# Optimization experiments

Hardware: AMD Instinct MI355X
Metric: run time of the kernel (lower is better)

## Reference

```python
import jax, jax.numpy as jnp
import numpy as np

D_MODEL = 1024
N_HEAD = 16
HEAD_DIM = D_MODEL // N_HEAD
B, T = 4, 1024
MIN_KEEP_H, MAX_KEEP_H = 2, 6


def setup_inputs() -> dict:
    key = jax.random.key(0)
    ks = jax.random.split(key, 8)
    x = jax.random.normal(ks[0], (B, T, D_MODEL), dtype=jnp.float32)
    # SignMaskLinear weight: uniform(-1, 1)
    q_w = jax.random.uniform(ks[1], (D_MODEL, D_MODEL), minval=-1.0, maxval=1.0, dtype=jnp.float32)
    # BitGhostLinear weights: randn
    k_w = jax.random.normal(ks[2], (D_MODEL, D_MODEL), dtype=jnp.float32)
    v_w = jax.random.normal(ks[3], (D_MODEL, D_MODEL), dtype=jnp.float32)
    o_w = jax.random.normal(ks[4], (D_MODEL, D_MODEL), dtype=jnp.float32)
    zeros = jnp.zeros((D_MODEL,), dtype=jnp.float32)
    return {"x": x, "q_w": q_w, "q_b": zeros, "k_w": k_w, "k_b": zeros,
            "v_w": v_w, "v_b": zeros, "o_w": o_w, "o_b": zeros}


def _ghost_attention(x, q_w, q_b, k_w, k_b, v_w, v_b, o_w, o_b):
    Bn, Tn, C = x.shape
    H, Dh = N_HEAD, HEAD_DIM
    # SignMaskLinear: effective weight is sign(w) * (w != 0)
    qw_eff = jnp.sign(q_w) * (q_w != 0).astype(x.dtype)
    q = (x @ qw_eff.T + q_b).reshape(Bn, Tn, H, Dh).transpose(0, 2, 1, 3)  # (B,H,T,Dh)
    k = (x @ k_w.T + k_b).reshape(Bn, Tn, H, Dh).transpose(0, 2, 1, 3)
    v = (x @ v_w.T + v_b).reshape(Bn, Tn, H, Dh).transpose(0, 2, 1, 3)
    # RMS-normalize q
    q = q / (jnp.sqrt(jnp.mean(q * q, axis=-1, keepdims=True)) + 1e-6)
    # Per-head top-k sparsification of q by |q| (static keep counts)
    ratios = np.linspace(0.35, 0.15, H)
    keep_counts = np.maximum((ratios * Dh).astype(np.int64), 1)  # trunc like .long()
    q_abs = jnp.abs(q)
    q_sorted = -jnp.sort(-q_abs, axis=-1)  # descending along Dh
    idx = jnp.asarray(keep_counts - 1, dtype=jnp.int32).reshape(1, H, 1, 1)
    thresh = jnp.take_along_axis(q_sorted, jnp.broadcast_to(idx, (Bn, H, Tn, 1)), axis=-1)
    q = q * (q_abs >= thresh).astype(q.dtype)
    # RMS-normalize k
    k = k / (jnp.sqrt(jnp.mean(k * k, axis=-1, keepdims=True)) + 1e-6)
    # Causal masked attention (no scale factor in original)
    logits = jnp.einsum('bhqd,bhkd->bhqk', q, k)
    causal = jnp.tril(jnp.ones((Tn, Tn), dtype=bool))
    logits = jnp.where(causal[None, None], logits, -jnp.inf)
    attn = jax.nn.softmax(logits, axis=-1)
    # Entropy-driven adaptive head pruning
    head_energy = jnp.mean(attn ** 2, axis=(2, 3))  # (B,H)
    head_prob = jax.nn.softmax(head_energy, axis=1)
    head_entropy = -jnp.sum(head_prob * jnp.log(head_prob + 1e-9), axis=1)  # (B,)
    ent_norm = jnp.clip(head_entropy / jnp.log(jnp.float32(H)), 0.0, 1.0)
    keep_h = jnp.round(MIN_KEEP_H + ent_norm * (MAX_KEEP_H - MIN_KEEP_H)).astype(jnp.int32)  # (B,)
    he_sorted = -jnp.sort(-head_energy, axis=1)  # descending (B,H)
    thresh_h = jnp.take_along_axis(he_sorted, (keep_h - 1)[:, None], axis=1)  # (B,1)
    head_mask = (head_energy >= thresh_h).astype(x.dtype)[:, :, None, None]  # (B,H,1,1)
    attn = attn * head_mask
    v = v * head_mask
    out = jnp.einsum('bhqk,bhkd->bhqd', attn, v).transpose(0, 2, 1, 3).reshape(Bn, Tn, C)
    return out @ o_w.T + o_b


def reference(x, q_w, q_b, k_w, k_b, v_w, v_b, o_w, o_b):
    return _ghost_attention(x, q_w, q_b, k_w, k_b, v_w, v_b, o_w, o_b)
```

## Files before the change

kernel.cpp:

```cpp
#include <hip/hip_runtime.h>
#include <math.h>

#define D_MODEL 1024
#define T_SEQ   1024
#define BATCH   4
#define NHEAD   16
#define HDIM    64

__constant__ int KEEPC[16] = {22,21,20,19,18,18,17,16,15,14,13,13,12,11,10,9};

typedef short bh8  __attribute__((ext_vector_type(8)));
typedef float f32x4 __attribute__((ext_vector_type(4)));
typedef int   i32x4 __attribute__((ext_vector_type(4)));

__device__ __forceinline__ unsigned short f2bf(float f) {
    unsigned int u = __float_as_uint(f);
    return (unsigned short)((u + 0x7FFFu + ((u >> 16) & 1u)) >> 16);
}
__device__ __forceinline__ float bf2f(unsigned short h) {
    return __uint_as_float(((unsigned int)h) << 16);
}

__global__ void cast_prep(const float* __restrict__ kw,
                          unsigned short* __restrict__ kwh,
                          unsigned short* __restrict__ kwl,
                          const float* __restrict__ vw,
                          unsigned short* __restrict__ vwb,
                          const float* __restrict__ ow,
                          unsigned short* __restrict__ owb,
                          const float* __restrict__ x,
                          signed char* __restrict__ dig,
                          unsigned short* __restrict__ xh,
                          unsigned short* __restrict__ xl,
                          const float* __restrict__ qw,
                          signed char* __restrict__ sg)
{
    const int NS = (D_MODEL * D_MODEL) / 8;
    const int NX = (BATCH * T_SEQ * D_MODEL) / 8;
    int i = blockIdx.x * 256 + threadIdx.x;

    if (i < 3 * NS) {
        const float* src; unsigned short* dh; unsigned short* dl = nullptr;
        long off;
        if (i < NS)          { src = kw; dh = kwh; dl = kwl; off = i; }
        else if (i < 2 * NS) { src = vw; dh = vwb; off = i - NS; }
        else                 { src = ow; dh = owb; off = i - 2 * NS; }
        long e = off * 8;
        alignas(16) float fl[8];
        *(float4*)&fl[0] = *(const float4*)(src + e);
        *(float4*)&fl[4] = *(const float4*)(src + e + 4);
        uint4 hp, lp;
        unsigned int* hpw = (unsigned int*)&hp;
        unsigned int* lpw = (unsigned int*)&lp;
        #pragma unroll
        for (int c = 0; c < 4; c++) {
            unsigned short h0 = f2bf(fl[2 * c]), h1 = f2bf(fl[2 * c + 1]);
            hpw[c] = (unsigned int)h0 | ((unsigned int)h1 << 16);
            if (dl) {
                unsigned short l0 = f2bf(fl[2 * c] - bf2f(h0));
                unsigned short l1 = f2bf(fl[2 * c + 1] - bf2f(h1));
                lpw[c] = (unsigned int)l0 | ((unsigned int)l1 << 16);
            }
        }
        *(uint4*)(dh + e) = hp;
        if (dl) *(uint4*)(dl + e) = lp;
    } else if (i < 3 * NS + NX) {
        long e = (long)(i - 3 * NS) * 8;
        alignas(16) float f[8];
        *(float4*)&f[0] = *(const float4*)(x + e);
        *(float4*)&f[4] = *(const float4*)(x + e + 4);
        signed char d[4][8];
        #pragma unroll
        for (int c = 0; c < 8; c++) {
            int n = (int)rintf(f[c] * 8388608.0f);
            int d0 = (signed char)(n & 0xff); n = (n - d0) >> 8;
            int d1 = (signed char)(n & 0xff); n = (n - d1) >> 8;
            int d2 = (signed char)(n & 0xff); n = (n - d2) >> 8;
            d[0][c] = (signed char)d0; d[1][c] = (signed char)d1;
            d[2][c] = (signed char)d2; d[3][c] = (signed char)n;
        }
        long row = e >> 10;
        int  kk  = (int)(e & 1023);
        long rt  = row >> 4;
        int  l15r = (int)(row & 15);
        int  kstep = kk >> 6;
        int  rg2 = (kk >> 4) & 3;
        int  L = rg2 * 16 + l15r;
        int  t = kk & 15;
        signed char* dp = dig + (rt << 16) + ((long)kstep << 12)
                              + ((long)L << 4) + t;
        #pragma unroll
        for (int p = 0; p < 4; p++)
            *(uint2*)(dp + (p << 10)) = *(uint2*)&d[p][0];
        uint4 hp, lp;
        unsigned int* hpw = (unsigned int*)&hp;
        unsigned int* lpw = (unsigned int*)&lp;
        #pragma unroll
        for (int c = 0; c < 4; c++) {
            unsigned short h0 = f2bf(f[2 * c]), h1 = f2bf(f[2 * c + 1]);
            hpw[c] = (unsigned int)h0 | ((unsigned int)h1 << 16);
            unsigned short l0 = f2bf(f[2 * c] - bf2f(h0));
            unsigned short l1 = f2bf(f[2 * c + 1] - bf2f(h1));
            lpw[c] = (unsigned int)l0 | ((unsigned int)l1 << 16);
        }
        *(uint4*)(xh + e) = hp;
        *(uint4*)(xl + e) = lp;
    } else if (i < 3 * NS + NX + NS) {
        long e = (long)(i - 3 * NS - NX) * 8;
        alignas(16) float f[8];
        *(float4*)&f[0] = *(const float4*)(qw + e);
        *(float4*)&f[4] = *(const float4*)(qw + e + 4);
        signed char s[8];
        #pragma unroll
        for (int c = 0; c < 8; c++)
            s[c] = (signed char)((f[c] > 0.f) - (f[c] < 0.f));
        long col = e >> 10;
        int  kk  = (int)(e & 1023);
        long ct  = col >> 4;
        int  l15c = (int)(col & 15);
        int  kstep = kk >> 6;
        int  rg2 = (kk >> 4) & 3;
        int  L = rg2 * 16 + l15c;
        int  t = kk & 15;
        signed char* sp = sg + (ct << 14) + ((long)kstep << 10)
                             + ((long)L << 4) + t;
        *(uint2*)sp = *(uint2*)&s[0];
    }
}

__global__ __launch_bounds__(256, 4) void gemm_q_i8(
    const signed char* __restrict__ dig, const signed char* __restrict__ sg,
    const float* __restrict__ Bi, unsigned short* __restrict__ Yq)
{
    int tid  = threadIdx.x;
    int blk  = blockIdx.x;
    int low  = blk & 7, rest = blk >> 3;
    int bn   = (rest & 15) * 64;
    int bm   = (((rest >> 4) << 3) + low) * 64;
    int wave = tid >> 6, lane = tid & 63;
    int l15  = lane & 15, rg = lane >> 4;

    int rt  = (bm >> 4) + wave;
    int ct0 = bn >> 4;

    i32x4 acc[4][4];
    #pragma unroll
    for (int p = 0; p < 4; p++)
        #pragma unroll
        for (int j = 0; j < 4; j++) acc[p][j] = (i32x4)0;

    const signed char* ar = dig + ((size_t)rt << 16) + (lane << 4);
    const signed char* br = sg + ((size_t)ct0 << 14) + (lane << 4);

    i32x4 aA[4], bA[4], aB[4], bB[4];
    #pragma unroll
    for (int p = 0; p < 4; p++) aA[p] = *(const i32x4*)(ar + (p << 10));
    #pragma unroll
    for (int j = 0; j < 4; j++) bA[j] = *(const i32x4*)(br + (j << 14));

    #pragma unroll
    for (int kk = 0; kk < 8; kk++) {
        #pragma unroll
        for (int p = 0; p < 4; p++) aB[p] = *(const i32x4*)(ar + 4096 + (p << 10));
        #pragma unroll
        for (int j = 0; j < 4; j++) bB[j] = *(const i32x4*)(br + 1024 + (j << 14));
        #pragma unroll
        for (int p = 0; p < 4; p++)
            #pragma unroll
            for (int j = 0; j < 4; j++)
                acc[p][j] = __builtin_amdgcn_mfma_i32_16x16x64_i8(
                    aA[p], bA[j], acc[p][j], 0, 0, 0);
        if (kk < 7) {
            #pragma unroll
            for (int p = 0; p < 4; p++) aA[p] = *(const i32x4*)(ar + 8192 + (p << 10));
            #pragma unroll
            for (int j = 0; j < 4; j++) bA[j] = *(const i32x4*)(br + 2048 + (j << 14));
        }
        #pragma unroll
        for (int p = 0; p < 4; p++)
            #pragma unroll
            for (int j = 0; j < 4; j++)
                acc[p][j] = __builtin_amdgcn_mfma_i32_16x16x64_i8(
                    aB[p], bB[j], acc[p][j], 0, 0, 0);
        ar += 8192; br += 2048;
    }

    int hh   = bn >> 6;
    int keep = KEEPC[hh];
    float bvj[4];
    #pragma unroll
    for (int j = 0; j < 4; j++) bvj[j] = Bi[bn + j * 16 + l15];

    float xv[4][4];
    #pragma unroll
    for (int j = 0; j < 4; j++)
        #pragma unroll
        for (int r = 0; r < 4; r++) {
            long t = (long)acc[0][j][r]
                   + ((long)acc[1][j][r] << 8)
                   + ((long)acc[2][j][r] << 16)
                   + ((long)acc[3][j][r] << 24);
            xv[j][r] = (float)((double)t * (1.0 / 8388608.0)) + bvj[j];
        }

    unsigned int shiftv = (unsigned int)(rg & 1) * 16;
    #pragma unroll
    for (int r = 0; r < 4; r++) {
        float ss = xv[0][r] * xv[0][r] + xv[1][r] * xv[1][r]
                 + xv[2][r] * xv[2][r] + xv[3][r] * xv[3][r];
        ss += __shfl_xor(ss, 1); ss += __shfl_xor(ss, 2);
        ss += __shfl_xor(ss, 4); ss += __shfl_xor(ss, 8);
        float rms = sqrtf(ss * (1.0f / 64.0f));

        float xn[4]; unsigned int ai[4];
        #pragma unroll
        for (int j = 0; j < 4; j++) {
            xn[j] = xv[j][r] / (rms + 1e-6f);
            ai[j] = __float_as_uint(fabsf(xn[j]));
        }

        unsigned int th = 0;
        for (int bit = 30; bit >= 0; --bit) {
            unsigned int cand = th | (1u << bit);
            int cnt = 0;
            #pragma unroll
            for (int j = 0; j < 4; j++) {
                unsigned long long bl = __ballot(ai[j] >= cand);
                unsigned int half = (rg & 2) ? (unsigned int)(bl >> 32)
                                             : (unsigned int)bl;
                cnt += __popc((half >> shiftv) & 0xFFFFu);
            }
            if (cnt >= keep) th = cand;
        }

        int row = bm + wave * 16 + rg * 4 + r;
        int bb = row >> 10, tt = row & 1023;
        unsigned int* qp32 = (unsigned int*)(Yq
            + (((size_t)(bb * NHEAD + hh)) * T_SEQ + tt) * 128);
        #pragma unroll
        for (int j = 0; j < 4; j++) {
            float o = (ai[j] < th) ? 0.f : xn[j];
            unsigned short hi = f2bf(o);
            unsigned short lo = f2bf(o - bf2f(hi));
            qp32[j * 16 + l15] = (unsigned int)hi | ((unsigned int)lo << 16);
        }
    }
}

#define GLDK 72

__global__ __launch_bounds__(256, 2) void gemm_kv(
    const unsigned short* __restrict__ xhg, const unsigned short* __restrict__ xlg,
    const unsigned short* __restrict__ kwh, const unsigned short* __restrict__ kwl,
    const float* __restrict__ kb,
    const unsigned short* __restrict__ vwb, const float* __restrict__ vb,
    unsigned short* __restrict__ Yk, unsigned short* __restrict__ Yv)
{
    __shared__ unsigned short Ah[128 * GLDK];
    __shared__ unsigned short Al[128 * GLDK];
    __shared__ unsigned short Whs[128 * GLDK];
    __shared__ unsigned short Wls[128 * GLDK];

    int tid  = threadIdx.x;
    int blk  = blockIdx.x;
    int z    = blk >> 8;
    int split = (z == 0);
    int inner = blk & 255;
    int low  = inner & 7, rest = inner >> 3;
    int bn   = (rest & 7) * 128;
    int bm   = (((rest >> 3) << 3) + low) * 128;
    const unsigned short* Wh = split ? kwh : vwb;
    const unsigned short* Wl = split ? kwl : vwb;
    const float*          Bi = split ? kb : vb;

    int wave = tid >> 6, lane = tid & 63;
    int l15  = lane & 15, q4 = lane >> 4;
    int wm   = (wave >> 1) * 64, wn = (wave & 1) * 64;
    int srow = tid >> 1;
    int scol = (tid & 1) * 32;

    f32x4 acc[4][4];
    #pragma unroll
    for (int i = 0; i < 4; i++)
        #pragma unroll
        for (int j = 0; j < 4; j++) acc[i][j] = (f32x4)0.f;

    const unsigned short* ahp = xhg + (size_t)(bm + srow) * D_MODEL + scol;
    const unsigned short* alp = xlg + (size_t)(bm + srow) * D_MODEL + scol;
    const unsigned short* whp = Wh + (size_t)(bn + srow) * D_MODEL + scol;
    const unsigned short* wlp = Wl + (size_t)(bn + srow) * D_MODEL + scol;

    uint4 a0, a1, a2, a3, g0, g1, g2, g3;
    uint4 w0, w1, w2, w3, x0, x1, x2, x3;
    a0 = *(const uint4*)(ahp + 0);  a1 = *(const uint4*)(ahp + 8);
    a2 = *(const uint4*)(ahp + 16); a3 = *(const uint4*)(ahp + 24);
    w0 = *(const uint4*)(whp + 0);  w1 = *(const uint4*)(whp + 8);
    w2 = *(const uint4*)(whp + 16); w3 = *(const uint4*)(whp + 24);
    if (split) {
        g0 = *(const uint4*)(alp + 0);  g1 = *(const uint4*)(alp + 8);
        g2 = *(const uint4*)(alp + 16); g3 = *(const uint4*)(alp + 24);
        x0 = *(const uint4*)(wlp + 0);  x1 = *(const uint4*)(wlp + 8);
        x2 = *(const uint4*)(wlp + 16); x3 = *(const uint4*)(wlp + 24);
    }

    for (int k0 = 0; k0 < D_MODEL; k0 += 64) {
        __syncthreads();
        unsigned short* as = &Ah[srow * GLDK + scol];
        *(uint4*)(as + 0) = a0; *(uint4*)(as + 8)  = a1;
        *(uint4*)(as + 16) = a2; *(uint4*)(as + 24) = a3;
        unsigned short* ws = &Whs[srow * GLDK + scol];
        *(uint4*)(ws + 0) = w0; *(uint4*)(ws + 8)  = w1;
        *(uint4*)(ws + 16) = w2; *(uint4*)(ws + 24) = w3;
        if (split) {
            unsigned short* als = &Al[srow * GLDK + scol];
            *(uint4*)(als + 0) = g0; *(uint4*)(als + 8)  = g1;
            *(uint4*)(als + 16) = g2; *(uint4*)(als + 24) = g3;
            unsigned short* wl2 = &Wls[srow * GLDK + scol];
            *(uint4*)(wl2 + 0) = x0; *(uint4*)(wl2 + 8)  = x1;
            *(uint4*)(wl2 + 16) = x2; *(uint4*)(wl2 + 24) = x3;
        }
        __syncthreads();

        if (k0 + 64 < D_MODEL) {
            ahp += 64; alp += 64; whp += 64; wlp += 64;
            a0 = *(const uint4*)(ahp + 0);  a1 = *(const uint4*)(ahp + 8);
            a2 = *(const uint4*)(ahp + 16); a3 = *(const uint4*)(ahp + 24);
            w0 = *(const uint4*)(whp + 0);  w1 = *(const uint4*)(whp + 8);
            w2 = *(const uint4*)(whp + 16); w3 = *(const uint4*)(whp + 24);
            if (split) {
                g0 = *(const uint4*)(alp + 0);  g1 = *(const uint4*)(alp + 8);
                g2 = *(const uint4*)(alp + 16); g3 = *(const uint4*)(alp + 24);
                x0 = *(const uint4*)(wlp + 0);  x1 = *(const uint4*)(wlp + 8);
                x2 = *(const uint4*)(wlp + 16); x3 = *(const uint4*)(wlp + 24);
            }
        }

        #pragma unroll
        for (int kc = 0; kc < 64; kc += 32) {
            bh8 ahf[4], whf[4];
            #pragma unroll
            for (int i = 0; i < 4; i++)
                ahf[i] = *(bh8*)&Ah[(wm + i * 16 + l15) * GLDK + kc + q4 * 8];
            #pragma unroll
            for (int j = 0; j < 4; j++)
                whf[j] = *(bh8*)&Whs[(wn + j * 16 + l15) * GLDK + kc + q4 * 8];
            #pragma unroll
            for (int i = 0; i < 4; i++)
                #pragma unroll
                for (int j = 0; j < 4; j++)
                    acc[i][j] = __builtin_amdgcn_mfma_f32_16x16x32_bf16(ahf[i], whf[j], acc[i][j], 0, 0, 0);
            if (split) {
                bh8 alf[4], wlf[4];
                #pragma unroll
                for (int i = 0; i < 4; i++)
                    alf[i] = *(bh8*)&Al[(wm + i * 16 + l15) * GLDK + kc + q4 * 8];
                #pragma unroll
                for (int j = 0; j < 4; j++)
                    wlf[j] = *(bh8*)&Wls[(wn + j * 16 + l15) * GLDK + kc + q4 * 8];
                #pragma unroll
                for (int i = 0; i < 4; i++)
                    #pragma unroll
                    for (int j = 0; j < 4; j++) {
                        acc[i][j] = __builtin_amdgcn_mfma_f32_16x16x32_bf16(ahf[i], wlf[j], acc[i][j], 0, 0, 0);
                        acc[i][j] = __builtin_amdgcn_mfma_f32_16x16x32_bf16(alf[i], whf[j], acc[i][j], 0, 0, 0);
                    }
            }
        }
    }

    if (split) {
        int hh = (bn + wn) >> 6;
        float bv[4];
        #pragma unroll
        for (int j = 0; j < 4; j++) bv[j] = Bi[bn + wn + j * 16 + l15];
        #pragma unroll
        for (int i = 0; i < 4; i++) {
            #pragma unroll
            for (int r = 0; r < 4; r++) {
                int row = bm + wm + i * 16 + q4 * 4 + r;
                int bb = row >> 10, tt = row & 1023;
                float vv[4]; float ss = 0.f;
                #pragma unroll
                for (int j = 0; j < 4; j++) {
                    vv[j] = acc[i][j][r] + bv[j];
                    ss += vv[j] * vv[j];
                }
                ss += __shfl_xor(ss, 1); ss += __shfl_xor(ss, 2);
                ss += __shfl_xor(ss, 4); ss += __shfl_xor(ss, 8);
                float rms = sqrtf(ss * (1.0f / 64.0f));
                unsigned short* kp = Yk + (((size_t)(bb * NHEAD + hh)) * T_SEQ + tt) * 128;
                #pragma unroll
                for (int j = 0; j < 4; j++) {
                    float xn = vv[j] / (rms + 1e-6f);
                    unsigned short hi = f2bf(xn);
                    unsigned short lo = f2bf(xn - bf2f(hi));
                    kp[j * 16 + l15]      = hi;
                    kp[64 + j * 16 + l15] = lo;
                }
            }
        }
    } else {
        #pragma unroll
        for (int j = 0; j < 4; j++) {
            int col = bn + wn + j * 16 + l15;
            int hh = col >> 6, dd = col & 63;
            float bvv = Bi[col];
            #pragma unroll
            for (int i = 0; i < 4; i++) {
                int row0 = bm + wm + i * 16 + q4 * 4;
                int bb = row0 >> 10, tt = row0 & 1023;
                uint2 u;
                u.x = (unsigned int)f2bf(acc[i][j][0] + bvv) | ((unsigned int)f2bf(acc[i][j][1] + bvv) << 16);
                u.y = (unsigned int)f2bf(acc[i][j][2] + bvv) | ((unsigned int)f2bf(acc[i][j][3] + bvv) << 16);
                *(uint2*)(Yv + ((size_t)(bb * NHEAD + hh) * HDIM + dd) * T_SEQ + tt) = u;
            }
        }
    }
}

#define KST 72

__global__ __launch_bounds__(256, 4) void attn_kernel(
    const unsigned short* __restrict__ Qsg,
    const unsigned short* __restrict__ Ksg,
    const unsigned short* __restrict__ Vtg,
    unsigned short* __restrict__ Ctx, double* __restrict__ He)
{
    __shared__ unsigned short Kh[64 * KST];
    __shared__ unsigned short Kl[64 * KST];
    __shared__ unsigned short Vt[64 * KST];
    __shared__ unsigned short Ps[4][16 * KST];

    int tid = threadIdx.x;
    int blk = blockIdx.x;
    int low = blk & 7, rest = blk >> 3;
    int v  = rest & 15;
    int mk = (rest >> 4) & 1;
    int k  = rest >> 5;
    int qt = (k == 0) ? v
           : (k == 1) ? (15 - v)
           : (k == 2) ? ((v + 4) & 15)
                      : ((11 - v) & 15);
    int h   = mk * 8 + low;
    int b   = k;
    int bh = b * NHEAD + h;
    size_t rbase = (size_t)bh * T_SEQ;

    int wave = tid >> 6, lane = tid & 63;
    int l15 = lane & 15, rg = lane >> 4;
    int srow = tid >> 2;
    int scol = (tid & 3) * 16;

    int qrow = qt * 64 + wave * 16 + l15;

    bh8 qf[2][2];
    {
        const unsigned int* qp32 = (const unsigned int*)(Qsg + (rbase + qrow) * 128);
        uint4 a = *(const uint4*)(qp32 + rg * 8);
        uint4 c = *(const uint4*)(qp32 + rg * 8 + 4);
        uint4 d = *(const uint4*)(qp32 + 32 + rg * 8);
        uint4 e = *(const uint4*)(qp32 + 32 + rg * 8 + 4);
        unsigned int hv[4], lv[4];
        hv[0] = __builtin_amdgcn_perm(a.y, a.x, 0x05040100u);
        hv[1] = __builtin_amdgcn_perm(a.w, a.z, 0x05040100u);
        hv[2] = __builtin_amdgcn_perm(c.y, c.x, 0x05040100u);
        hv[3] = __builtin_amdgcn_perm(c.w, c.z, 0x05040100u);
        lv[0] = __builtin_amdgcn_perm(a.y, a.x, 0x07060302u);
        lv[1] = __builtin_amdgcn_perm(a.w, a.z, 0x07060302u);
        lv[2] = __builtin_amdgcn_perm(c.y, c.x, 0x07060302u);
        lv[3] = __builtin_amdgcn_perm(c.w, c.z, 0x07060302u);
        qf[0][0] = *(bh8*)hv;
        qf[1][0] = *(bh8*)lv;
        hv[0] = __builtin_amdgcn_perm(d.y, d.x, 0x05040100u);
        hv[1] = __builtin_amdgcn_perm(d.w, d.z, 0x05040100u);
        hv[2] = __builtin_amdgcn_perm(e.y, e.x, 0x05040100u);
        hv[3] = __builtin_amdgcn_perm(e.w, e.z, 0x05040100u);
        lv[0] = __builtin_amdgcn_perm(d.y, d.x, 0x07060302u);
        lv[1] = __builtin_amdgcn_perm(d.w, d.z, 0x07060302u);
        lv[2] = __builtin_amdgcn_perm(e.y, e.x, 0x07060302u);
        lv[3] = __builtin_amdgcn_perm(e.w, e.z, 0x07060302u);
        qf[0][1] = *(bh8*)hv;
        qf[1][1] = *(bh8*)lv;
    }

    float m = -1e30f, l = 0.f, s2 = 0.f;
    f32x4 o[4];
    #pragma unroll
    for (int n = 0; n < 4; n++) o[n] = (f32x4)0.f;

    unsigned short* myPs = &Ps[wave][0];
    const unsigned short* vbase = Vtg + (size_t)bh * HDIM * T_SEQ;

    for (int kt = 0; kt <= qt; ++kt) {
        const unsigned short* krow = Ksg + (rbase + kt * 64 + srow) * 128;
        uint4 kh0 = *(const uint4*)(krow + scol);
        uint4 kh1 = *(const uint4*)(krow + scol + 8);
        uint4 kl0 = *(const uint4*)(krow + 64 + scol);
        uint4 kl1 = *(const uint4*)(krow + 64 + scol + 8);
        const unsigned short* vrow = vbase + (size_t)srow * T_SEQ + kt * 64 + scol;
        uint4 vv0 = *(const uint4*)(vrow);
        uint4 vv1 = *(const uint4*)(vrow + 8);

        __syncthreads();
        *(uint4*)&Kh[srow * KST + scol]     = kh0;
        *(uint4*)&Kh[srow * KST + scol + 8] = kh1;
        *(uint4*)&Kl[srow * KST + scol]     = kl0;
        *(uint4*)&Kl[srow * KST + scol + 8] = kl1;
        *(uint4*)&Vt[srow * KST + scol]     = vv0;
        *(uint4*)&Vt[srow * KST + scol + 8] = vv1;
        __syncthreads();

        f32x4 s[4];
        #pragma unroll
        for (int n = 0; n < 4; n++) s[n] = (f32x4)0.f;
        #pragma unroll
        for (int n = 0; n < 4; n++) {
            const unsigned short* kr = &Kh[(n * 16 + l15) * KST + rg * 8];
            const unsigned short* lr = &Kl[(n * 16 + l15) * KST + rg * 8];
            bh8 ah0 = *(const bh8*)(kr);
            bh8 ah1 = *(const bh8*)(kr + 32);
            bh8 al0 = *(const bh8*)(lr);
            bh8 al1 = *(const bh8*)(lr + 32);
            s[n] = __builtin_amdgcn_mfma_f32_16x16x32_bf16(ah0, qf[0][0], s[n], 0, 0, 0);
            s[n] = __builtin_amdgcn_mfma_f32_16x16x32_bf16(ah1, qf[0][1], s[n], 0, 0, 0);
            s[n] = __builtin_amdgcn_mfma_f32_16x16x32_bf16(ah0, qf[1][0], s[n], 0, 0, 0);
            s[n] = __builtin_amdgcn_mfma_f32_16x16x32_bf16(ah1, qf[1][1], s[n], 0, 0, 0);
            s[n] = __builtin_amdgcn_mfma_f32_16x16x32_bf16(al0, qf[0][0], s[n], 0, 0, 0);
            s[n] = __builtin_amdgcn_mfma_f32_16x16x32_bf16(al1, qf[0][1], s[n], 0, 0, 0);
        }

        if (kt == qt) {
            #pragma unroll
            for (int n = 0; n < 4; n++)
                #pragma unroll
                for (int e2 = 0; e2 < 4; e2++)
                    if (n * 16 + rg * 4 + e2 > wave * 16 + l15) s[n][e2] = -1e30f;
        }

        float mx = -1e30f;
        #pragma unroll
        for (int n = 0; n < 4; n++)
            #pragma unroll
            for (int e2 = 0; e2 < 4; e2++) mx = fmaxf(mx, s[n][e2]);
        mx = fmaxf(mx, __shfl_xor(mx, 16));
        mx = fmaxf(mx, __shfl_xor(mx, 32));
        float mn = fmaxf(m, mx);
        float alpha = __expf(m - mn);
        m = mn;
        float rs = 0.f, rs2 = 0.f;
        #pragma unroll
        for (int n = 0; n < 4; n++)
            #pragma unroll
            for (int e2 = 0; e2 < 4; e2++) {
                float pv = __expf(s[n][e2] - mn);
                s[n][e2] = pv;
                rs += pv; rs2 += pv * pv;
            }
        rs  += __shfl_xor(rs, 16);  rs  += __shfl_xor(rs, 32);
        rs2 += __shfl_xor(rs2, 16); rs2 += __shfl_xor(rs2, 32);
        l  = l * alpha + rs;
        s2 = s2 * alpha * alpha + rs2;

        #pragma unroll
        for (int n = 0; n < 4; n++) {
            uint2 u;
            u.x = (unsigned int)f2bf(s[n][0]) | ((unsigned int)f2bf(s[n][1]) << 16);
            u.y = (unsigned int)f2bf(s[n][2]) | ((unsigned int)f2bf(s[n][3]) << 16);
            *(uint2*)&myPs[l15 * KST + n * 16 + rg * 4] = u;
        }
        bh8 pf0 = *(bh8*)&myPs[l15 * KST + rg * 8];
        bh8 pf1 = *(bh8*)&myPs[l15 * KST + 32 + rg * 8];

        #pragma unroll
        for (int n = 0; n < 4; n++) {
            o[n] *= alpha;
            const unsigned short* vr = &Vt[(n * 16 + l15) * KST + rg * 8];
            bh8 v0 = *(const bh8*)(vr);
            bh8 v1 = *(const bh8*)(vr + 32);
            o[n] = __builtin_amdgcn_mfma_f32_16x16x32_bf16(v0, pf0, o[n], 0, 0, 0);
            o[n] = __builtin_amdgcn_mfma_f32_16x16x32_bf16(v1, pf1, o[n], 0, 0, 0);
        }
    }

    float linv = 1.f / l;
    float en = (rg == 0) ? s2 * linv * linv : 0.f;
    en += __shfl_xor(en, 1); en += __shfl_xor(en, 2);
    en += __shfl_xor(en, 4); en += __shfl_xor(en, 8);
    if (lane == 0) atomicAdd(&He[bh], (double)en);

    unsigned short* cp = Ctx + ((size_t)b * T_SEQ + qrow) * D_MODEL + h * HDIM;
    #pragma unroll
    for (int n = 0; n < 4; n++) {
        uint2 u;
        u.x = (unsigned int)f2bf(o[n][0] * linv) | ((unsigned int)f2bf(o[n][1] * linv) << 16);
        u.y = (unsigned int)f2bf(o[n][2] * linv) | ((unsigned int)f2bf(o[n][3] * linv) << 16);
        *(uint2*)(cp + n * 16 + rg * 4) = u;
    }
}

__global__ __launch_bounds__(256, 2) void gemm_obf(
    const unsigned short* __restrict__ A, const unsigned short* __restrict__ W,
    const float* __restrict__ Bi, float* __restrict__ Y,
    const double* __restrict__ He)
{
    __shared__ unsigned short As[128 * GLDK];
    __shared__ unsigned short Ws[128 * GLDK];
    __shared__ double hs[34];
    __shared__ float maskS[NHEAD];

    int tid  = threadIdx.x;
    int blk  = blockIdx.x;
    int low  = blk & 7, rest = blk >> 3;
    int bn   = (rest & 7) * 128;
    int bm   = (((rest >> 3) << 3) + low) * 128;
    int batch = bm >> 10;

    if (tid < NHEAD) hs[tid] = He[batch * NHEAD + tid] * (1.0 / (1024.0 * 1024.0));
    __syncthreads();
    if (tid < NHEAD) {
        double mx = hs[0];
        for (int h2 = 1; h2 < NHEAD; h2++) mx = fmax(mx, hs[h2]);
        hs[NHEAD + tid] = exp(hs[tid] - mx);
    }
    __syncthreads();
    if (tid == 0) {
        double s = 0.0;
        for (int h2 = 0; h2 < NHEAD; h2++) s += hs[NHEAD + h2];
        hs[32] = s;
    }
    __syncthreads();
    if (tid < NHEAD) {
        double ph = hs[NHEAD + tid] / hs[32];
        hs[NHEAD + tid] = ph * log(ph + 1e-9);
    }
    __syncthreads();
    if (tid == 0) {
        double ent = 0.0;
        for (int h2 = 0; h2 < NHEAD; h2++) ent -= hs[NHEAD + h2];
        double entn = ent / log(16.0);
        entn = fmin(fmax(entn, 0.0), 1.0);
        int keep = (int)rint(2.0 + entn * 4.0);
        if (keep < 1) keep = 1;
        if (keep > NHEAD) keep = NHEAD;
        double srt[NHEAD];
        for (int h2 = 0; h2 < NHEAD; h2++) srt[h2] = hs[h2];
        for (int i = 1; i < NHEAD; i++) {
            double v = srt[i]; int j = i - 1;
            while (j >= 0 && srt[j] < v) { srt[j + 1] = srt[j]; j--; }
            srt[j + 1] = v;
        }
        double th = srt[keep - 1];
        for (int h2 = 0; h2 < NHEAD; h2++)
            maskS[h2] = (hs[h2] >= th) ? 1.0f : 0.0f;
    }
    __syncthreads();

    int wave = tid >> 6, lane = tid & 63;
    int l15  = lane & 15, q4 = lane >> 4;
    int wm   = (wave >> 1) * 64, wn = (wave & 1) * 64;
    int srow = tid >> 1;
    int scol = (tid & 1) * 32;

    f32x4 acc[4][4];
    #pragma unroll
    for (int i = 0; i < 4; i++)
        #pragma unroll
        for (int j = 0; j < 4; j++) acc[i][j] = (f32x4)0.f;

    const unsigned short* ap = A + (size_t)(bm + srow) * D_MODEL + scol;
    const unsigned short* wp = W + (size_t)(bn + srow) * D_MODEL + scol;

    for (int k0 = 0; k0 < D_MODEL; k0 += 64) {
        if (maskS[k0 >> 6] == 0.f) { ap += 64; wp += 64; continue; }

        uint4 a0 = *(const uint4*)(ap + 0),  a1 = *(const uint4*)(ap + 8);
        uint4 a2 = *(const uint4*)(ap + 16), a3 = *(const uint4*)(ap + 24);
        uint4 w0 = *(const uint4*)(wp + 0),  w1 = *(const uint4*)(wp + 8);
        uint4 w2 = *(const uint4*)(wp + 16), w3 = *(const uint4*)(wp + 24);
        ap += 64; wp += 64;
        __syncthreads();
        unsigned short* as = &As[srow * GLDK + scol];
        *(uint4*)(as + 0) = a0; *(uint4*)(as + 8)  = a1;
        *(uint4*)(as + 16) = a2; *(uint4*)(as + 24) = a3;
        unsigned short* ws = &Ws[srow * GLDK + scol];
        *(uint4*)(ws + 0) = w0; *(uint4*)(ws + 8)  = w1;
        *(uint4*)(ws + 16) = w2; *(uint4*)(ws + 24) = w3;
        __syncthreads();

        #pragma unroll
        for (int kc = 0; kc < 64; kc += 32) {
            bh8 af[4], wf[4];
            #pragma unroll
            for (int i = 0; i < 4; i++)
                af[i] = *(bh8*)&As[(wm + i * 16 + l15) * GLDK + kc + q4 * 8];
            #pragma unroll
            for (int j = 0; j < 4; j++)
                wf[j] = *(bh8*)&Ws[(wn + j * 16 + l15) * GLDK + kc + q4 * 8];
            #pragma unroll
            for (int i = 0; i < 4; i++)
                #pragma unroll
                for (int j = 0; j < 4; j++)
                    acc[i][j] = __builtin_amdgcn_mfma_f32_16x16x32_bf16(af[i], wf[j], acc[i][j], 0, 0, 0);
        }
    }

    #pragma unroll
    for (int j = 0; j < 4; j++) {
        int col = bn + wn + j * 16 + l15;
        float bv = Bi[col];
        #pragma unroll
        for (int i = 0; i < 4; i++) {
            int row = bm + wm + i * 16 + q4 * 4;
            #pragma unroll
            for (int r = 0; r < 4; r++)
                Y[(size_t)(row + r) * D_MODEL + col] = acc[i][j][r] + bv;
        }
    }
}

extern "C" void kernel_launch(void* const* d_in, const int* in_sizes, int n_in,
                              void* d_out, int out_size, void* d_ws, size_t ws_size,
                              hipStream_t stream)
{
    (void)in_sizes; (void)n_in; (void)out_size; (void)ws_size;
    const float* x  = (const float*)d_in[0];
    const float* qw = (const float*)d_in[1];
    const float* qb = (const float*)d_in[2];
    const float* kw = (const float*)d_in[3];
    const float* kb = (const float*)d_in[4];
    const float* vw = (const float*)d_in[5];
    const float* vb = (const float*)d_in[6];
    const float* ow = (const float*)d_in[7];
    const float* ob = (const float*)d_in[8];
    float* out = (float*)d_out;

    char* base = (char*)d_ws;
    const size_t MB = (size_t)1024 * 1024;
    unsigned short* qbf  = (unsigned short*)(base);
    unsigned short* kbf  = (unsigned short*)(base + 16 * MB);
    unsigned short* vt   = (unsigned short*)(base + 32 * MB);
    unsigned short* ctxb = (unsigned short*)(base + 40 * MB);
    signed char*    dig  = (signed char*)(base + 32 * MB);
    unsigned short* kwh  = (unsigned short*)(base + 48 * MB);
    unsigned short* kwl  = (unsigned short*)(base + 50 * MB);
    unsigned short* vwb  = (unsigned short*)(base + 52 * MB);
    unsigned short* owb  = (unsigned short*)(base + 54 * MB);
    signed char*    sg   = (signed char*)(base + 56 * MB);
    double*         he   = (double*)(base + 57 * MB);
    unsigned short* xh   = (unsigned short*)(base + 58 * MB);
    unsigned short* xl   = (unsigned short*)(base + 66 * MB);

    hipMemsetAsync(he, 0, 64 * sizeof(double), stream);

    cast_prep<<<4096, 256, 0, stream>>>(kw, kwh, kwl, vw, vwb, ow, owb,
                                        x, dig, xh, xl, qw, sg);
    gemm_q_i8<<<1024, 256, 0, stream>>>(dig, sg, qb, qbf);
    gemm_kv<<<512, 256, 0, stream>>>(xh, xl, kwh, kwl, kb, vwb, vb, kbf, vt);
    attn_kernel<<<1024, 256, 0, stream>>>(qbf, kbf, vt, ctxb, he);
    gemm_obf<<<256, 256, 0, stream>>>(ctxb, owb, ob, out, he);
}
```

Before: 239.9 us.

## Rebalance K/V projection GEMM so each block computes both K and V tiles

The fused K/V projection kernel used to give half the blocks the split-precision K tile (three MFMA passes) and the other half the single-pass V tile. That made the grid unbalanced, with K blocks setting the critical path. Now every block handles a 128x64 output tile and computes K and then V for the same columns, so all blocks do equal work. The cost is a narrower tile, which means less operand reuse and loading the x tile twice per block. The output GEMM's LDS stride constant is renamed without changing its value.

```diff
diff --git a/kernel.cpp b/kernel.cpp
--- a/kernel.cpp
+++ b/kernel.cpp
@@ -258,123 +258,107 @@
 {
     __shared__ unsigned short Ah[128 * GLDK];
     __shared__ unsigned short Al[128 * GLDK];
-    __shared__ unsigned short Whs[128 * GLDK];
-    __shared__ unsigned short Wls[128 * GLDK];
+    __shared__ unsigned short Whs[64 * GLDK];
+    __shared__ unsigned short Wls[64 * GLDK];
 
     int tid  = threadIdx.x;
     int blk  = blockIdx.x;
-    int z    = blk >> 8;
-    int split = (z == 0);
-    int inner = blk & 255;
-    int low  = inner & 7, rest = inner >> 3;
-    int bn   = (rest & 7) * 128;
-    int bm   = (((rest >> 3) << 3) + low) * 128;
-    const unsigned short* Wh = split ? kwh : vwb;
-    const unsigned short* Wl = split ? kwl : vwb;
-    const float*          Bi = split ? kb : vb;
+    int low  = blk & 7, rest = blk >> 3;
+    int bn   = (rest & 15) * 64;
+    int bm   = (((rest >> 4) << 3) + low) * 128;
 
     int wave = tid >> 6, lane = tid & 63;
     int l15  = lane & 15, q4 = lane >> 4;
-    int wm   = (wave >> 1) * 64, wn = (wave & 1) * 64;
+    int wm   = wave * 32;
     int srow = tid >> 1;
     int scol = (tid & 1) * 32;
-
-    f32x4 acc[4][4];
-    #pragma unroll
-    for (int i = 0; i < 4; i++)
-        #pragma unroll
-        for (int j = 0; j < 4; j++) acc[i][j] = (f32x4)0.f;
+    int wrow = tid >> 2;
+    int wcol = (tid & 3) * 16;
 
     const unsigned short* ahp = xhg + (size_t)(bm + srow) * D_MODEL + scol;
     const unsigned short* alp = xlg + (size_t)(bm + srow) * D_MODEL + scol;
-    const unsigned short* whp = Wh + (size_t)(bn + srow) * D_MODEL + scol;
-    const unsigned short* wlp = Wl + (size_t)(bn + srow) * D_MODEL + scol;
-
-    uint4 a0, a1, a2, a3, g0, g1, g2, g3;
-    uint4 w0, w1, w2, w3, x0, x1, x2, x3;
-    a0 = *(const uint4*)(ahp + 0);  a1 = *(const uint4*)(ahp + 8);
-    a2 = *(const uint4*)(ahp + 16); a3 = *(const uint4*)(ahp + 24);
-    w0 = *(const uint4*)(whp + 0);  w1 = *(const uint4*)(whp + 8);
-    w2 = *(const uint4*)(whp + 16); w3 = *(const uint4*)(whp + 24);
-    if (split) {
-        g0 = *(const uint4*)(alp + 0);  g1 = *(const uint4*)(alp + 8);
-        g2 = *(const uint4*)(alp + 16); g3 = *(const uint4*)(alp + 24);
+
+    {
+        f32x4 acc[2][4];
+        #pragma unroll
+        for (int i = 0; i < 2; i++)
+            #pragma unroll
+            for (int j = 0; j < 4; j++) acc[i][j] = (f32x4)0.f;
+
+        const unsigned short* whp = kwh + (size_t)(bn + wrow) * D_MODEL + wcol;
+        const unsigned short* wlp = kwl + (size_t)(bn + wrow) * D_MODEL + wcol;
+        const unsigned short* ah1 = ahp;
+        const unsigned short* al1 = alp;
+
+        uint4 a0, a1, a2, a3, g0, g1, g2, g3, w0, w1, x0, x1;
+        a0 = *(const uint4*)(ah1 + 0);  a1 = *(const uint4*)(ah1 + 8);
+        a2 = *(const uint4*)(ah1 + 16); a3 = *(const uint4*)(ah1 + 24);
+        g0 = *(const uint4*)(al1 + 0);  g1 = *(const uint4*)(al1 + 8);
+        g2 = *(const uint4*)(al1 + 16); g3 = *(const uint4*)(al1 + 24);
+        w0 = *(const uint4*)(whp + 0);  w1 = *(const uint4*)(whp + 8);
         x0 = *(const uint4*)(wlp + 0);  x1 = *(const uint4*)(wlp + 8);
-        x2 = *(const uint4*)(wlp + 16); x3 = *(const uint4*)(wlp + 24);
-    }
-
-    for (int k0 = 0; k0 < D_MODEL; k0 += 64) {
-        __syncthreads();
-        unsigned short* as = &Ah[srow * GLDK + scol];
-        *(uint4*)(as + 0) = a0; *(uint4*)(as + 8)  = a1;
-        *(uint4*)(as + 16) = a2; *(uint4*)(as + 24) = a3;
-        unsigned short* ws = &Whs[srow * GLDK + scol];
-        *(uint4*)(ws + 0) = w0; *(uint4*)(ws + 8)  = w1;
-        *(uint4*)(ws + 16) = w2; *(uint4*)(ws + 24) = w3;
-        if (split) {
+
+        for (int k0 = 0; k0 < D_MODEL; k0 += 64) {
+            __syncthreads();
+            unsigned short* as = &Ah[srow * GLDK + scol];
+            *(uint4*)(as + 0) = a0; *(uint4*)(as + 8)  = a1;
+            *(uint4*)(as + 16) = a2; *(uint4*)(as + 24) = a3;
             unsigned short* als = &Al[srow * GLDK + scol];
             *(uint4*)(als + 0) = g0; *(uint4*)(als + 8)  = g1;
             *(uint4*)(als + 16) = g2; *(uint4*)(als + 24) = g3;
-            unsigned short* wl2 = &Wls[srow * GLDK + scol];
-            *(uint4*)(wl2 + 0) = x0; *(uint4*)(wl2 + 8)  = x1;
-            *(uint4*)(wl2 + 16) = x2; *(uint4*)(wl2 + 24) = x3;
-        }
-        __syncthreads();
-
-        if (k0 + 64 < D_MODEL) {
-            ahp += 64; alp += 64; whp += 64; wlp += 64;
-            a0 = *(const uint4*)(ahp + 0);  a1 = *(const uint4*)(ahp + 8);
-            a2 = *(const uint4*)(ahp + 16); a3 = *(const uint4*)(ahp + 24);
-            w0 = *(const uint4*)(whp + 0);  w1 = *(const uint4*)(whp + 8);
-            w2 = *(const uint4*)(whp + 16); w3 = *(const uint4*)(whp + 24);
-            if (split) {
-                g0 = *(const uint4*)(alp + 0);  g1 = *(const uint4*)(alp + 8);
-                g2 = *(const uint4*)(alp + 16); g3 = *(const uint4*)(alp + 24);
+            unsigned short* ws = &Whs[wrow * GLDK + wcol];
+            *(uint4*)(ws + 0) = w0; *(uint4*)(ws + 8) = w1;
+            unsigned short* wl2 = &Wls[wrow * GLDK + wcol];
+            *(uint4*)(wl2 + 0) = x0; *(uint4*)(wl2 + 8) = x1;
+            __syncthreads();
+
+            if (k0 + 64 < D_MODEL) {
+                ah1 += 64; al1 += 64; whp += 64; wlp += 64;
+                a0 = *(const uint4*)(ah1 + 0);  a1 = *(const uint4*)(ah1 + 8);
+                a2 = *(const uint4*)(ah1 + 16); a3 = *(const uint4*)(ah1 + 24);
+                g0 = *(const uint4*)(al1 + 0);  g1 = *(const uint4*)(al1 + 8);
+                g2 = *(const uint4*)(al1 + 16); g3 = *(const uint4*)(al1 + 24);
+                w0 = *(const uint4*)(whp + 0);  w1 = *(const uint4*)(whp + 8);
                 x0 = *(const uint4*)(wlp + 0);  x1 = *(const uint4*)(wlp + 8);
-                x2 = *(const uint4*)(wlp + 16); x3 = *(const uint4*)(wlp + 24);
-            }
-        }
-
-        #pragma unroll
-        for (int kc = 0; kc < 64; kc += 32) {
-            bh8 ahf[4], whf[4];
-            #pragma unroll
-            for (int i = 0; i < 4; i++)
-                ahf[i] = *(bh8*)&Ah[(wm + i * 16 + l15) * GLDK + kc + q4 * 8];
-            #pragma unroll
-            for (int j = 0; j < 4; j++)
-                whf[j] = *(bh8*)&Whs[(wn + j * 16 + l15) * GLDK + kc + q4 * 8];
-            #pragma unroll
-            for (int i = 0; i < 4; i++)
-                #pragma unroll
-                for (int j = 0; j < 4; j++)
-                    acc[i][j] = __builtin_amdgcn_mfma_f32_16x16x32_bf16(ahf[i], whf[j], acc[i][j], 0, 0, 0);
-            if (split) {
-                bh8 alf[4], wlf[4];
-                #pragma unroll
-                for (int i = 0; i < 4; i++)
+            }
+
+            #pragma unroll
+            for (int kc = 0; kc < 64; kc += 32) {
+                bh8 ahf[2], alf[2], whf[4], wlf[4];
+                #pragma unroll
+                for (int i = 0; i < 2; i++) {
+                    ahf[i] = *(bh8*)&Ah[(wm + i * 16 + l15) * GLDK + kc + q4 * 8];
                     alf[i] = *(bh8*)&Al[(wm + i * 16 + l15) * GLDK + kc + q4 * 8];
-                #pragma unroll
-                for (int j = 0; j < 4; j++)
-                    wlf[j] = *(bh8*)&Wls[(wn + j * 16 + l15) * GLDK + kc + q4 * 8];
-                #pragma unroll
-                for (int i = 0; i < 4; i++)
+                }
+                #pragma unroll
+                for (int j = 0; j < 4; j++) {
+                    whf[j] = *(bh8*)&Whs[(j * 16 + l15) * GLDK + kc + q4 * 8];
+                    wlf[j] = *(bh8*)&Wls[(j * 16 + l15) * GLDK + kc + q4 * 8];
+                }
+                #pragma unroll
+                for (int i = 0; i < 2; i++)
+                    #pragma unroll
+                    for (int j = 0; j < 4; j++)
+                        acc[i][j] = __builtin_amdgcn_mfma_f32_16x16x32_bf16(
+                            ahf[i], whf[j], acc[i][j], 0, 0, 0);
+                #pragma unroll
+                for (int i = 0; i < 2; i++)
                     #pragma unroll
                     for (int j = 0; j < 4; j++) {
-                        acc[i][j] = __builtin_amdgcn_mfma_f32_16x16x32_bf16(ahf[i], wlf[j], acc[i][j], 0, 0, 0);
-                        acc[i][j] = __builtin_amdgcn_mfma_f32_16x16x32_bf16(alf[i], whf[j], acc[i][j], 0, 0, 0);
+                        acc[i][j] = __builtin_amdgcn_mfma_f32_16x16x32_bf16(
+                            ahf[i], wlf[j], acc[i][j], 0, 0, 0);
+                        acc[i][j] = __builtin_amdgcn_mfma_f32_16x16x32_bf16(
+                            alf[i], whf[j], acc[i][j], 0, 0, 0);
                     }
             }
         }
-    }
-
-    if (split) {
-        int hh = (bn + wn) >> 6;
+
+        int hh = bn >> 6;
         float bv[4];
         #pragma unroll
-        for (int j = 0; j < 4; j++) bv[j] = Bi[bn + wn + j * 16 + l15];
-        #pragma unroll
-        for (int i = 0; i < 4; i++) {
+        for (int j = 0; j < 4; j++) bv[j] = kb[bn + j * 16 + l15];
+        #pragma unroll
+        for (int i = 0; i < 2; i++) {
             #pragma unroll
             for (int r = 0; r < 4; r++) {
                 int row = bm + wm + i * 16 + q4 * 4 + r;
@@ -399,19 +383,71 @@
                 }
             }
         }
-    } else {
+    }
+
+    {
+        f32x4 acc[2][4];
+        #pragma unroll
+        for (int i = 0; i < 2; i++)
+            #pragma unroll
+            for (int j = 0; j < 4; j++) acc[i][j] = (f32x4)0.f;
+
+        const unsigned short* whp = vwb + (size_t)(bn + wrow) * D_MODEL + wcol;
+        const unsigned short* ah2 = ahp;
+
+        uint4 a0, a1, a2, a3, w0, w1;
+        a0 = *(const uint4*)(ah2 + 0);  a1 = *(const uint4*)(ah2 + 8);
+        a2 = *(const uint4*)(ah2 + 16); a3 = *(const uint4*)(ah2 + 24);
+        w0 = *(const uint4*)(whp + 0);  w1 = *(const uint4*)(whp + 8);
+
+        for (int k0 = 0; k0 < D_MODEL; k0 += 64) {
+            __syncthreads();
+            unsigned short* as = &Ah[srow * GLDK + scol];
+            *(uint4*)(as + 0) = a0; *(uint4*)(as + 8)  = a1;
+            *(uint4*)(as + 16) = a2; *(uint4*)(as + 24) = a3;
+            unsigned short* ws = &Whs[wrow * GLDK + wcol];
+            *(uint4*)(ws + 0) = w0; *(uint4*)(ws + 8) = w1;
+            __syncthreads();
+
+            if (k0 + 64 < D_MODEL) {
+                ah2 += 64; whp += 64;
+                a0 = *(const uint4*)(ah2 + 0);  a1 = *(const uint4*)(ah2 + 8);
+                a2 = *(const uint4*)(ah2 + 16); a3 = *(const uint4*)(ah2 + 24);
+                w0 = *(const uint4*)(whp + 0);  w1 = *(const uint4*)(whp + 8);
+            }
+
+            #pragma unroll
+            for (int kc = 0; kc < 64; kc += 32) {
+                bh8 ahf[2], whf[4];
+                #pragma unroll
+                for (int i = 0; i < 2; i++)
+                    ahf[i] = *(bh8*)&Ah[(wm + i * 16 + l15) * GLDK + kc + q4 * 8];
+                #pragma unroll
+                for (int j = 0; j < 4; j++)
+                    whf[j] = *(bh8*)&Whs[(j * 16 + l15) * GLDK + kc + q4 * 8];
+                #pragma unroll
+                for (int i = 0; i < 2; i++)
+                    #pragma unroll
+                    for (int j = 0; j < 4; j++)
+                        acc[i][j] = __builtin_amdgcn_mfma_f32_16x16x32_bf16(
+                            ahf[i], whf[j], acc[i][j], 0, 0, 0);
+            }
+        }
+
         #pragma unroll
         for (int j = 0; j < 4; j++) {
-            int col = bn + wn + j * 16 + l15;
+            int col = bn + j * 16 + l15;
             int hh = col >> 6, dd = col & 63;
-            float bvv = Bi[col];
-            #pragma unroll
-            for (int i = 0; i < 4; i++) {
+            float bvv = vb[col];
+            #pragma unroll
+            for (int i = 0; i < 2; i++) {
                 int row0 = bm + wm + i * 16 + q4 * 4;
                 int bb = row0 >> 10, tt = row0 & 1023;
                 uint2 u;
-                u.x = (unsigned int)f2bf(acc[i][j][0] + bvv) | ((unsigned int)f2bf(acc[i][j][1] + bvv) << 16);
-                u.y = (unsigned int)f2bf(acc[i][j][2] + bvv) | ((unsigned int)f2bf(acc[i][j][3] + bvv) << 16);
+                u.x = (unsigned int)f2bf(acc[i][j][0] + bvv)
+                    | ((unsigned int)f2bf(acc[i][j][1] + bvv) << 16);
+                u.y = (unsigned int)f2bf(acc[i][j][2] + bvv)
+                    | ((unsigned int)f2bf(acc[i][j][3] + bvv) << 16);
                 *(uint2*)(Yv + ((size_t)(bb * NHEAD + hh) * HDIM + dd) * T_SEQ + tt) = u;
             }
         }
@@ -598,13 +634,15 @@
     }
 }
 
+#define GLDO 72
+
 __global__ __launch_bounds__(256, 2) void gemm_obf(
     const unsigned short* __restrict__ A, const unsigned short* __restrict__ W,
     const float* __restrict__ Bi, float* __restrict__ Y,
     const double* __restrict__ He)
 {
-    __shared__ unsigned short As[128 * GLDK];
-    __shared__ unsigned short Ws[128 * GLDK];
+    __shared__ unsigned short As[128 * GLDO];
+    __shared__ unsigned short Ws[128 * GLDO];
     __shared__ double hs[34];
     __shared__ float maskS[NHEAD];
 
@@ -679,10 +717,10 @@
         uint4 w2 = *(const uint4*)(wp + 16), w3 = *(const uint4*)(wp + 24);
         ap += 64; wp += 64;
         __syncthreads();
-        unsigned short* as = &As[srow * GLDK + scol];
+        unsigned short* as = &As[srow * GLDO + scol];
         *(uint4*)(as + 0) = a0; *(uint4*)(as + 8)  = a1;
         *(uint4*)(as + 16) = a2; *(uint4*)(as + 24) = a3;
-        unsigned short* ws = &Ws[srow * GLDK + scol];
+        unsigned short* ws = &Ws[srow * GLDO + scol];
         *(uint4*)(ws + 0) = w0; *(uint4*)(ws + 8)  = w1;
         *(uint4*)(ws + 16) = w2; *(uint4*)(ws + 24) = w3;
         __syncthreads();
@@ -692,10 +730,10 @@
             bh8 af[4], wf[4];
             #pragma unroll
             for (int i = 0; i < 4; i++)
-                af[i] = *(bh8*)&As[(wm + i * 16 + l15) * GLDK + kc + q4 * 8];
+                af[i] = *(bh8*)&As[(wm + i * 16 + l15) * GLDO + kc + q4 * 8];
             #pragma unroll
             for (int j = 0; j < 4; j++)
-                wf[j] = *(bh8*)&Ws[(wn + j * 16 + l15) * GLDK + kc + q4 * 8];
+                wf[j] = *(bh8*)&Ws[(wn + j * 16 + l15) * GLDO + kc + q4 * 8];
             #pragma unroll
             for (int i = 0; i < 4; i++)
                 #pragma unroll
```

Measured after the change: 252.1 us. 5.1% more time.
